# Performance work log

Measured on AMD Instinct MI355X. Metric: run time of the kernel, lower is better.

Reference implementation:

```python
import jax, jax.numpy as jnp
import numpy as np
from jax.ops import segment_sum, segment_max

N, E = 50000, 500000
D_IN, D_H, D_OUT = 128, 256, 40
BN_EPS = 1e-5


def setup_inputs() -> dict:
    key = jax.random.key(0)
    ks = jax.random.split(key, 16)
    g = lambda k, shape, fan: jax.random.normal(k, shape, jnp.float32) * (1.0 / np.sqrt(fan))
    inp = {
        "x": jax.random.normal(ks[0], (N, D_IN), jnp.float32),
        "edge_index": jax.random.randint(ks[1], (2, E), 0, N, jnp.int64),
        # GAT (heads=1)
        "W_gat": g(ks[2], (D_IN, D_H), D_IN),
        "att_src": g(ks[3], (D_H,), D_H),
        "att_dst": g(ks[4], (D_H,), D_H),
        "b_gat": jnp.zeros((D_H,), jnp.float32),
        # GIN MLP
        "W_gin1": g(ks[5], (D_IN, D_H), D_IN),
        "b_gin1": jnp.zeros((D_H,), jnp.float32),
        "W_gin2": g(ks[6], (D_H, D_H), D_H),
        "b_gin2": jnp.zeros((D_H,), jnp.float32),
        # GCN
        "W_gcn": g(ks[7], (D_IN, D_H), D_IN),
        "b_gcn": jnp.zeros((D_H,), jnp.float32),
        # BatchNorm1d(3*hidden)
        "gamma": jnp.ones((3 * D_H,), jnp.float32),
        "beta": jnp.zeros((3 * D_H,), jnp.float32),
        # head
        "W_lin": g(ks[8], (3 * D_H, D_H), 3 * D_H),
        "b_lin": jnp.zeros((D_H,), jnp.float32),
        "W_lin2": g(ks[9], (D_H, D_OUT), D_H),
        "b_lin2": jnp.zeros((D_OUT,), jnp.float32),
    }
    return inp


def _forward(x, edge_index, W_gat, att_src, att_dst, b_gat, W_gin1, b_gin1,
             W_gin2, b_gin2, W_gcn, b_gcn, gamma, beta, W_lin, b_lin, W_lin2, b_lin2):
    n = x.shape[0]
    src, dst = edge_index[0], edge_index[1]
    loop = jnp.arange(n, dtype=src.dtype)
    src_sl = jnp.concatenate([src, loop])  # edges + self-loops (GAT/GCN)
    dst_sl = jnp.concatenate([dst, loop])

    # ---- GATConv (1 head), messages src -> dst, softmax over dst ----
    xs = x @ W_gat                                   # [N, H]
    a = jax.nn.leaky_relu(xs @ att_src, negative_slope=0.2) if False else None
    e = (xs @ att_src)[src_sl] + (xs @ att_dst)[dst_sl]   # [E+N]
    e = jax.nn.leaky_relu(e, negative_slope=0.2)
    m = segment_max(e, dst_sl, num_segments=n)
    w = jnp.exp(e - m[dst_sl])
    denom = segment_sum(w, dst_sl, num_segments=n)
    alpha = w / denom[dst_sl]
    x_gat = segment_sum(alpha[:, None] * xs[src_sl], dst_sl, num_segments=n) + b_gat

    # ---- GINConv (eps=0): MLP(x + sum_neighbors x_j) ----
    agg = segment_sum(x[src], dst, num_segments=n)
    h = x + agg
    x_gin = jax.nn.relu(h @ W_gin1 + b_gin1) @ W_gin2 + b_gin2

    # ---- GCNConv: symmetric normalization with self-loops ----
    deg = segment_sum(jnp.ones_like(dst_sl, dtype=x.dtype), dst_sl, num_segments=n)
    dis = jax.lax.rsqrt(jnp.maximum(deg, 1.0))  # deg >= 1 due to self-loops
    norm = dis[src_sl] * dis[dst_sl]
    xw = x @ W_gcn
    x_gcn = segment_sum(norm[:, None] * xw[src_sl], dst_sl, num_segments=n) + b_gcn

    # ---- concat -> BN (training-mode batch stats) -> ReLU -> MLP head ----
    xc = jnp.concatenate([x_gat, x_gin, x_gcn], axis=1)  # [N, 3H]
    mu = jnp.mean(xc, axis=0)
    var = jnp.mean((xc - mu) ** 2, axis=0)
    xb = (xc - mu) * jax.lax.rsqrt(var + BN_EPS) * gamma + beta
    h2 = jax.nn.relu(jax.nn.relu(xb) @ W_lin + b_lin)
    return h2 @ W_lin2 + b_lin2


def reference(x, edge_index, W_gat, att_src, att_dst, b_gat, W_gin1, b_gin1,
              W_gin2, b_gin2, W_gcn, b_gcn, gamma, beta, W_lin, b_lin, W_lin2, b_lin2):
    return _forward(x, edge_index, W_gat, att_src, att_dst, b_gat, W_gin1, b_gin1,
                    W_gin2, b_gin2, W_gcn, b_gcn, gamma, beta, W_lin, b_lin, W_lin2, b_lin2)
```

## Files before the change

kernel.cpp:

```cpp
#include <hip/hip_runtime.h>
#include <math.h>

#define NN 50000
#define NE 500000
#define NRB 391

typedef __attribute__((ext_vector_type(8))) short short8;
typedef __attribute__((ext_vector_type(4))) float f32x4;

__device__ __forceinline__ float leaky02(float x) { return x > 0.f ? x : 0.2f * x; }
__device__ __forceinline__ ushort f2b(float f) {
    uint u = __float_as_uint(f);
    u += 0x7fffu + ((u >> 16) & 1u);
    return (ushort)(u >> 16);
}
__device__ __forceinline__ float b2f(ushort h) { return __uint_as_float(((uint)h) << 16); }
__device__ __forceinline__ float b2f_lo(uint w) { return __uint_as_float(w << 16); }
__device__ __forceinline__ float b2f_hi(uint w) { return __uint_as_float(w & 0xffff0000u); }
__device__ __forceinline__ uint pack2(float a, float b) {
    return (uint)f2b(a) | ((uint)f2b(b) << 16);
}

__global__ void mm_wt_all(const float* __restrict__ Wg, const float* __restrict__ Wi1,
                          const float* __restrict__ Wi2, const float* __restrict__ Wc,
                          const float* __restrict__ Wl,
                          ushort* __restrict__ tg, ushort* __restrict__ ti1,
                          ushort* __restrict__ ti2, ushort* __restrict__ tc,
                          ushort* __restrict__ tl)
{
    int idx = blockIdx.x * 256 + threadIdx.x;
    const float* W; ushort* T; int K; int base;
    if (idx < 32768)       { W = Wg;  T = tg;  K = 128; base = 0; }
    else if (idx < 65536)  { W = Wi1; T = ti1; K = 128; base = 32768; }
    else if (idx < 131072) { W = Wi2; T = ti2; K = 256; base = 65536; }
    else if (idx < 163840) { W = Wc;  T = tc;  K = 128; base = 131072; }
    else if (idx < 360448) { W = Wl;  T = tl;  K = 768; base = 163840; }
    else return;
    int i = idx - base;
    int n = i / K, k = i - n * K;
    T[i] = f2b(W[(size_t)k * 256 + n]);
}

__global__ void mm_attvec(const float* __restrict__ W, const float* __restrict__ as_,
                          const float* __restrict__ ad_, float* __restrict__ va, float* __restrict__ vd)
{
    int i = threadIdx.x;
    const float* vec = (i < 128) ? as_ : ad_;
    int k = i & 127;
    float s = 0.f;
    for (int j = 0; j < 256; ++j) s += W[(size_t)k * 256 + j] * vec[j];
    if (i < 128) va[k] = s; else vd[k] = s;
}

__global__ __launch_bounds__(256) void mm_cvt_es(const float* __restrict__ x,
                                                 const float* __restrict__ va, const float* __restrict__ vd,
                                                 ushort* __restrict__ xb,
                                                 float* __restrict__ es, float* __restrict__ ed)
{
    int node = blockIdx.x * 4 + (threadIdx.x >> 6);
    int lane = threadIdx.x & 63;
    if (node >= NN) return;
    float2 xv = *(const float2*)(x + (size_t)node * 128 + lane * 2);
    float2 a = *(const float2*)(va + lane * 2);
    float2 b = *(const float2*)(vd + lane * 2);
    *(uint*)(xb + (size_t)node * 128 + lane * 2) = pack2(xv.x, xv.y);
    float s = xv.x * a.x + xv.y * a.y;
    float d = xv.x * b.x + xv.y * b.y;
    #pragma unroll
    for (int off = 32; off; off >>= 1) {
        s += __shfl_down(s, off);
        d += __shfl_down(d, off);
    }
    if (lane == 0) { es[node] = s; ed[node] = d; }
}

__global__ void mm_count(const int* __restrict__ dst, int* __restrict__ deg)
{
    int e = blockIdx.x * 256 + threadIdx.x;
    if (e >= NE) return;
    atomicAdd(&deg[dst[e]], 1);
}

__global__ __launch_bounds__(256) void mm_scan1(const int* __restrict__ deg, int* __restrict__ part)
{
    __shared__ int red[256];
    int i = blockIdx.x * 256 + threadIdx.x;
    red[threadIdx.x] = (i < NN) ? deg[i] : 0;
    __syncthreads();
    for (int off = 128; off; off >>= 1) {
        if (threadIdx.x < off) red[threadIdx.x] += red[threadIdx.x + off];
        __syncthreads();
    }
    if (threadIdx.x == 0) part[blockIdx.x] = red[0];
}

__global__ __launch_bounds__(256) void mm_scan2(int* __restrict__ part, int nb)
{
    __shared__ int tile[256];
    int t = threadIdx.x;
    int v = (t < nb) ? part[t] : 0;
    tile[t] = v; __syncthreads();
    for (int off = 1; off < 256; off <<= 1) {
        int a = (t >= off) ? tile[t - off] : 0;
        __syncthreads();
        tile[t] += a;
        __syncthreads();
    }
    if (t < nb) part[t] = tile[t] - v;
}

__global__ __launch_bounds__(256) void mm_scan3(const int* __restrict__ deg, const int* __restrict__ part,
                                                int* __restrict__ row_ptr, int* __restrict__ cursor)
{
    __shared__ int tile[256];
    int t = threadIdx.x;
    int i = blockIdx.x * 256 + t;
    int v = (i < NN) ? deg[i] : 0;
    tile[t] = v; __syncthreads();
    for (int off = 1; off < 256; off <<= 1) {
        int a = (t >= off) ? tile[t - off] : 0;
        __syncthreads();
        tile[t] += a;
        __syncthreads();
    }
    if (i < NN) {
        int ex = part[blockIdx.x] + tile[t] - v;
        row_ptr[i] = ex;
        cursor[i] = ex;
    }
    if (i == 0) row_ptr[NN] = NE;
}

__global__ void mm_fill(const int* __restrict__ src, const int* __restrict__ dst,
                        int* __restrict__ cursor, int* __restrict__ csr_src)
{
    int e = blockIdx.x * 256 + threadIdx.x;
    if (e >= NE) return;
    int pos = atomicAdd(&cursor[dst[e]], 1);
    csr_src[pos] = src[e];
}

__global__ __launch_bounds__(256) void mm_sortseg(const int* __restrict__ row_ptr, int* __restrict__ csr_src)
{
    int d = blockIdx.x * 4 + (threadIdx.x >> 6);
    int lane = threadIdx.x & 63;
    if (d >= NN) return;
    int start = row_ptr[d], end = row_ptr[d + 1];
    int deg = end - start;
    if (deg <= 1 || deg > 64) return;
    int v = (start + lane < end) ? csr_src[start + lane] : 0x7fffffff;
    #pragma unroll
    for (int k = 2; k <= 64; k <<= 1) {
        #pragma unroll
        for (int j = k >> 1; j > 0; j >>= 1) {
            int o = __shfl_xor(v, j);
            bool asc = ((lane & k) == 0);
            bool low = ((lane & j) == 0);
            v = (asc == low) ? min(v, o) : max(v, o);
        }
    }
    if (start + lane < end) csr_src[start + lane] = v;
}

__global__ void mm_dis(const int* __restrict__ row_ptr, float* __restrict__ dis)
{
    int i = blockIdx.x * 256 + threadIdx.x;
    if (i >= NN) return;
    dis[i] = rsqrtf((float)(row_ptr[i + 1] - row_ptr[i] + 1));
}

__global__ __launch_bounds__(256) void mm_node_agg(
    const int* __restrict__ row_ptr, const int* __restrict__ csr_src,
    const float* __restrict__ es, const float* __restrict__ ed,
    const float* __restrict__ dis,
    const ushort* __restrict__ xb, ushort* __restrict__ aggb)
{
    int d = blockIdx.x * 4 + (threadIdx.x >> 6);
    int lane = threadIdx.x & 63;
    if (d >= NN) return;
    int start = row_ptr[d], end = row_ptr[d + 1];
    float edd = ed[d], disd = dis[d];
    float selfv = leaky02(es[d] + edd);

    int myidx = -1; float myl = -3.0e38f, mynw = 0.f;
    if (start + lane < end) {
        myidx = csr_src[start + lane];
        myl = leaky02(es[myidx] + edd);
        mynw = dis[myidx] * disd;
    }
    float lmax = fmaxf(selfv, myl);
    for (int e = start + 64 + lane; e < end; e += 64)
        lmax = fmaxf(lmax, leaky02(es[csr_src[e]] + edd));
    #pragma unroll
    for (int off = 1; off < 64; off <<= 1) lmax = fmaxf(lmax, __shfl_xor(lmax, off));
    float m = lmax;

    float lsum = (myidx >= 0) ? __expf(myl - m) : 0.f;
    if (lane == 0) lsum += __expf(selfv - m);
    for (int e = start + 64 + lane; e < end; e += 64)
        lsum += __expf(leaky02(es[csr_src[e]] + edd) - m);
    #pragma unroll
    for (int off = 1; off < 64; off <<= 1) lsum += __shfl_xor(lsum, off);
    float inv = 1.f / lsum;
    float myal = __expf(myl - m) * inv;

    float aself = __expf(selfv - m) * inv;
    float d2 = disd * disd;
    uint wself = *(const uint*)(xb + (size_t)d * 128 + lane * 2);
    float x0 = b2f_lo(wself), x1 = b2f_hi(wself);
    float gat0 = aself * x0, gat1 = aself * x1;
    float gin0 = x0, gin1 = x1;
    float gcn0 = d2 * x0, gcn1 = d2 * x1;

    for (int base = start; base < end; base += 64) {
        int cnt = min(64, end - base);
        int bidx; float bal, bnw;
        if (base == start) { bidx = myidx; bal = myal; bnw = mynw; }
        else {
            bidx = -1; bal = 0.f; bnw = 0.f;
            if (base + lane < end) {
                bidx = csr_src[base + lane];
                bal = __expf(leaky02(es[bidx] + edd) - m) * inv;
                bnw = dis[bidx] * disd;
            }
        }
        int j = 0;
        for (; j + 4 <= cnt; j += 4) {
            int   s0 = __shfl(bidx, j),     s1 = __shfl(bidx, j + 1);
            int   s2 = __shfl(bidx, j + 2), s3 = __shfl(bidx, j + 3);
            float a0 = __shfl(bal, j),      a1 = __shfl(bal, j + 1);
            float a2 = __shfl(bal, j + 2),  a3 = __shfl(bal, j + 3);
            float n0 = __shfl(bnw, j),      n1 = __shfl(bnw, j + 1);
            float n2 = __shfl(bnw, j + 2),  n3 = __shfl(bnw, j + 3);
            uint w0 = *(const uint*)(xb + (size_t)s0 * 128 + lane * 2);
            uint w1 = *(const uint*)(xb + (size_t)s1 * 128 + lane * 2);
            uint w2 = *(const uint*)(xb + (size_t)s2 * 128 + lane * 2);
            uint w3 = *(const uint*)(xb + (size_t)s3 * 128 + lane * 2);
            float p0, p1;
            p0 = b2f_lo(w0); p1 = b2f_hi(w0);
            gat0 += a0 * p0; gat1 += a0 * p1; gin0 += p0; gin1 += p1; gcn0 += n0 * p0; gcn1 += n0 * p1;
            p0 = b2f_lo(w1); p1 = b2f_hi(w1);
            gat0 += a1 * p0; gat1 += a1 * p1; gin0 += p0; gin1 += p1; gcn0 += n1 * p0; gcn1 += n1 * p1;
            p0 = b2f_lo(w2); p1 = b2f_hi(w2);
            gat0 += a2 * p0; gat1 += a2 * p1; gin0 += p0; gin1 += p1; gcn0 += n2 * p0; gcn1 += n2 * p1;
            p0 = b2f_lo(w3); p1 = b2f_hi(w3);
            gat0 += a3 * p0; gat1 += a3 * p1; gin0 += p0; gin1 += p1; gcn0 += n3 * p0; gcn1 += n3 * p1;
        }
        for (; j < cnt; ++j) {
            int   s0 = __shfl(bidx, j);
            float a0 = __shfl(bal, j);
            float n0 = __shfl(bnw, j);
            uint w0 = *(const uint*)(xb + (size_t)s0 * 128 + lane * 2);
            float p0 = b2f_lo(w0), p1 = b2f_hi(w0);
            gat0 += a0 * p0; gat1 += a0 * p1; gin0 += p0; gin1 += p1; gcn0 += n0 * p0; gcn1 += n0 * p1;
        }
    }
    ushort* orow = aggb + (size_t)d * 384;
    *(uint*)(orow + lane * 2)       = pack2(gat0, gat1);
    *(uint*)(orow + 128 + lane * 2) = pack2(gin0, gin1);
    *(uint*)(orow + 256 + lane * 2) = pack2(gcn0, gcn1);
}

__device__ __forceinline__ void gemm_core(
    const ushort* __restrict__ A, int lda, const ushort* __restrict__ Bt,
    const float* __restrict__ bias, float* __restrict__ pstat, int colbase,
    ushort* __restrict__ Cb, int ldc, int M, int K, int relu,
    ushort* lds)
{
    const int tid = threadIdx.x;
    const int wave = tid >> 6, lane = tid & 63;
    const int row0 = blockIdx.x * 128;
    const int col0 = blockIdx.y * 128;

    int arow0 = min(row0 + wave * 16 + (lane >> 2), M - 1);
    int arow1 = min(row0 + 64 + wave * 16 + (lane >> 2), M - 1);
    int brow0 = col0 + wave * 16 + (lane >> 2);
    int brow1 = col0 + 64 + wave * 16 + (lane >> 2);
    const ushort* pa0 = A + (size_t)arow0 * lda + (lane & 3) * 8;
    const ushort* pa1 = A + (size_t)arow1 * lda + (lane & 3) * 8;
    const ushort* pb0 = Bt + (size_t)brow0 * K + (lane & 3) * 8;
    const ushort* pb1 = Bt + (size_t)brow1 * K + (lane & 3) * 8;
    const int wr = (wave >> 1) * 64, wc = (wave & 1) * 64;

    f32x4 zero = {0.f, 0.f, 0.f, 0.f};
    f32x4 acc[4][4];
    #pragma unroll
    for (int m = 0; m < 4; ++m)
        #pragma unroll
        for (int n = 0; n < 4; ++n) acc[m][n] = zero;

    const int nt = K >> 5;

#define STAGE_C(bufi) { \
    ushort* Lb = lds + (bufi) * 8192; \
    __builtin_amdgcn_global_load_lds((const __attribute__((address_space(1))) void*)pa0, \
        (__attribute__((address_space(3))) void*)(Lb + wave * 512), 16, 0, 0); \
    __builtin_amdgcn_global_load_lds((const __attribute__((address_space(1))) void*)pa1, \
        (__attribute__((address_space(3))) void*)(Lb + 2048 + wave * 512), 16, 0, 0); \
    __builtin_amdgcn_global_load_lds((const __attribute__((address_space(1))) void*)pb0, \
        (__attribute__((address_space(3))) void*)(Lb + 4096 + wave * 512), 16, 0, 0); \
    __builtin_amdgcn_global_load_lds((const __attribute__((address_space(1))) void*)pb1, \
        (__attribute__((address_space(3))) void*)(Lb + 6144 + wave * 512), 16, 0, 0); \
    pa0 += 32; pa1 += 32; pb0 += 32; pb1 += 32; }

    STAGE_C(0);
    for (int t = 0; t < nt; ++t) {
        int cur = t & 1;
        if (t + 1 < nt) {
            STAGE_C(cur ^ 1);
            asm volatile("s_waitcnt vmcnt(4) lgkmcnt(0)" ::: "memory");
        } else {
            asm volatile("s_waitcnt vmcnt(0) lgkmcnt(0)" ::: "memory");
        }
        __builtin_amdgcn_s_barrier();
        const ushort* As = lds + cur * 8192;
        const ushort* Bs = As + 4096;
        short8 a[4], b[4];
        #pragma unroll
        for (int m = 0; m < 4; ++m)
            a[m] = *(const short8*)&As[(wr + m * 16 + (lane & 15)) * 32 + (lane >> 4) * 8];
        #pragma unroll
        for (int n = 0; n < 4; ++n)
            b[n] = *(const short8*)&Bs[(wc + n * 16 + (lane & 15)) * 32 + (lane >> 4) * 8];
        #pragma unroll
        for (int m = 0; m < 4; ++m)
            #pragma unroll
            for (int n = 0; n < 4; ++n)
                acc[m][n] = __builtin_amdgcn_mfma_f32_16x16x32_bf16(a[m], b[n], acc[m][n], 0, 0, 0);
        if (t + 1 < nt) __builtin_amdgcn_s_barrier();
    }
#undef STAGE_C

    #pragma unroll
    for (int n = 0; n < 4; ++n) {
        int col = col0 + wc + n * 16 + (lane & 15);
        float bb = bias ? bias[col] : 0.f;
        float s_acc = 0.f, q_acc = 0.f;
        #pragma unroll
        for (int m = 0; m < 4; ++m) {
            int rb = row0 + wr + m * 16 + (lane >> 4) * 4;
            #pragma unroll
            for (int r = 0; r < 4; ++r) {
                int row = rb + r;
                if (row < M) {
                    float v = acc[m][n][r] + bb;
                    if (relu) v = fmaxf(v, 0.f);
                    Cb[(size_t)row * ldc + col] = f2b(v);
                    s_acc += v; q_acc += v * v;
                }
            }
        }
        if (pstat) {
            s_acc += __shfl_xor(s_acc, 16); q_acc += __shfl_xor(q_acc, 16);
            s_acc += __shfl_xor(s_acc, 32); q_acc += __shfl_xor(q_acc, 32);
            if (lane < 16) {
                size_t slot = (size_t)(colbase + col) * NRB + blockIdx.x;
                unsafeAtomicAdd(&pstat[slot], s_acc);
                unsafeAtomicAdd(&pstat[(size_t)768 * NRB + slot], q_acc);
            }
        }
    }
}

__global__ __launch_bounds__(256) void mm_gemm3(
    const ushort* __restrict__ aggb,
    const ushort* __restrict__ wt_gat, const ushort* __restrict__ wt_gin1, const ushort* __restrict__ wt_gcn,
    const float* __restrict__ b_gat, const float* __restrict__ b_gin1, const float* __restrict__ b_gcn,
    float* __restrict__ pstat,
    ushort* __restrict__ xcb, ushort* __restrict__ hid_b)
{
    __shared__ ushort lds[16384];
    if (blockIdx.z == 0)
        gemm_core(aggb,       384, wt_gat,  b_gat,  pstat,   0,   xcb,       768, NN, 128, 0, lds);
    else if (blockIdx.z == 1)
        gemm_core(aggb + 128, 384, wt_gin1, b_gin1, nullptr, 0,   hid_b,     256, NN, 128, 1, lds);
    else
        gemm_core(aggb + 256, 384, wt_gcn,  b_gcn,  pstat,   512, xcb + 512, 768, NN, 128, 0, lds);
}

__global__ __launch_bounds__(256) void mm_gemm_bf(
    const ushort* __restrict__ A, int lda, const ushort* __restrict__ Bt,
    const float* __restrict__ bias, float* __restrict__ pstat, int colbase,
    ushort* __restrict__ Cb, int ldc, int M, int K, int relu)
{
    __shared__ ushort lds[16384];
    gemm_core(A, lda, Bt, bias, pstat, colbase, Cb, ldc, M, K, relu, lds);
}

__device__ __forceinline__ uint4 bn_relu_pack_l(uint4 w, const float* sc, const float* sh, int c)
{
    uint4 o;
    o.x = pack2(fmaxf(b2f_lo(w.x) * sc[c + 0] + sh[c + 0], 0.f), fmaxf(b2f_hi(w.x) * sc[c + 1] + sh[c + 1], 0.f));
    o.y = pack2(fmaxf(b2f_lo(w.y) * sc[c + 2] + sh[c + 2], 0.f), fmaxf(b2f_hi(w.y) * sc[c + 3] + sh[c + 3], 0.f));
    o.z = pack2(fmaxf(b2f_lo(w.z) * sc[c + 4] + sh[c + 4], 0.f), fmaxf(b2f_hi(w.z) * sc[c + 5] + sh[c + 5], 0.f));
    o.w = pack2(fmaxf(b2f_lo(w.w) * sc[c + 6] + sh[c + 6], 0.f), fmaxf(b2f_hi(w.w) * sc[c + 7] + sh[c + 7], 0.f));
    return o;
}

__global__ __launch_bounds__(256) void mm_gemm_bn(
    const ushort* __restrict__ A, const ushort* __restrict__ Bt,
    const float* __restrict__ bias,
    const float* __restrict__ sc, const float* __restrict__ sh,
    ushort* __restrict__ Cb, int ldc, int M)
{
    const int K = 768, lda = 768;
    __shared__ ushort lds[16384];
    __shared__ float sc_l[768], sh_l[768];
    const int tid = threadIdx.x;
    for (int i = tid; i < 768; i += 256) { sc_l[i] = sc[i]; sh_l[i] = sh[i]; }

    const int wave = tid >> 6, lane = tid & 63;
    const int row0 = blockIdx.x * 128;
    const int col0 = blockIdx.y * 128;

    int arow0 = min(row0 + wave * 16 + (lane >> 2), M - 1);
    int arow1 = min(row0 + 64 + wave * 16 + (lane >> 2), M - 1);
    int brow0 = col0 + wave * 16 + (lane >> 2);
    int brow1 = col0 + 64 + wave * 16 + (lane >> 2);
    const ushort* pa0 = A + (size_t)arow0 * lda + (lane & 3) * 8;
    const ushort* pa1 = A + (size_t)arow1 * lda + (lane & 3) * 8;
    const ushort* pb0 = Bt + (size_t)brow0 * K + (lane & 3) * 8;
    const ushort* pb1 = Bt + (size_t)brow1 * K + (lane & 3) * 8;
    const int wr = (wave >> 1) * 64, wc = (wave & 1) * 64;

    f32x4 zero = {0.f, 0.f, 0.f, 0.f};
    f32x4 acc[4][4];
    #pragma unroll
    for (int m = 0; m < 4; ++m)
        #pragma unroll
        for (int n = 0; n < 4; ++n) acc[m][n] = zero;

    const int nt = K >> 5;

#define STAGE_B(bufi) { \
    ushort* Lb = lds + (bufi) * 8192; \
    __builtin_amdgcn_global_load_lds((const __attribute__((address_space(1))) void*)pb0, \
        (__attribute__((address_space(3))) void*)(Lb + 4096 + wave * 512), 16, 0, 0); \
    __builtin_amdgcn_global_load_lds((const __attribute__((address_space(1))) void*)pb1, \
        (__attribute__((address_space(3))) void*)(Lb + 6144 + wave * 512), 16, 0, 0); \
    pb0 += 32; pb1 += 32; }

    uint4 w0 = *(const uint4*)pa0, w1 = *(const uint4*)pa1;
    pa0 += 32; pa1 += 32;
    STAGE_B(0);
    __syncthreads();
    {
        int c = (lane & 3) * 8;
        *(uint4*)(lds + wave * 512 + lane * 8) = bn_relu_pack_l(w0, sc_l, sh_l, c);
        *(uint4*)(lds + 2048 + wave * 512 + lane * 8) = bn_relu_pack_l(w1, sc_l, sh_l, c);
    }

    for (int t = 0; t < nt; ++t) {
        int cur = t & 1;
        bool more = (t + 1 < nt);
        uint4 w0n, w1n;
        if (more) {
            w0n = *(const uint4*)pa0; w1n = *(const uint4*)pa1;
            pa0 += 32; pa1 += 32;
            STAGE_B(cur ^ 1);
            asm volatile("s_waitcnt vmcnt(4) lgkmcnt(0)" ::: "memory");
        } else {
            asm volatile("s_waitcnt vmcnt(0) lgkmcnt(0)" ::: "memory");
        }
        __builtin_amdgcn_s_barrier();
        const ushort* As = lds + cur * 8192;
        const ushort* Bs = As + 4096;
        short8 a[4], b[4];
        #pragma unroll
        for (int m = 0; m < 4; ++m)
            a[m] = *(const short8*)&As[(wr + m * 16 + (lane & 15)) * 32 + (lane >> 4) * 8];
        #pragma unroll
        for (int n = 0; n < 4; ++n)
            b[n] = *(const short8*)&Bs[(wc + n * 16 + (lane & 15)) * 32 + (lane >> 4) * 8];
        #pragma unroll
        for (int m = 0; m < 4; ++m)
            #pragma unroll
            for (int n = 0; n < 4; ++n)
                acc[m][n] = __builtin_amdgcn_mfma_f32_16x16x32_bf16(a[m], b[n], acc[m][n], 0, 0, 0);
        if (more) {
            int c = (t + 1) * 32 + (lane & 3) * 8;
            ushort* Ln = lds + (cur ^ 1) * 8192;
            *(uint4*)(Ln + wave * 512 + lane * 8) = bn_relu_pack_l(w0n, sc_l, sh_l, c);
            *(uint4*)(Ln + 2048 + wave * 512 + lane * 8) = bn_relu_pack_l(w1n, sc_l, sh_l, c);
            __builtin_amdgcn_s_barrier();
        }
    }
#undef STAGE_B

    #pragma unroll
    for (int n = 0; n < 4; ++n) {
        int col = col0 + wc + n * 16 + (lane & 15);
        float bb = bias[col];
        #pragma unroll
        for (int m = 0; m < 4; ++m) {
            int rb = row0 + wr + m * 16 + (lane >> 4) * 4;
            #pragma unroll
            for (int r = 0; r < 4; ++r) {
                int row = rb + r;
                if (row < M)
                    Cb[(size_t)row * ldc + col] = f2b(fmaxf(acc[m][n][r] + bb, 0.f));
            }
        }
    }
}

__global__ void mm_bn_fin(const float* __restrict__ pstat, const float* __restrict__ gamma,
                          const float* __restrict__ beta,
                          float* __restrict__ scale, float* __restrict__ shift)
{
    int c = blockIdx.x * 256 + threadIdx.x;
    if (c >= 768) return;
    const float* ps = pstat + (size_t)c * NRB;
    const float* pq = pstat + (size_t)768 * NRB + (size_t)c * NRB;
    float s = 0.f, q = 0.f;
    for (int rb = 0; rb < NRB; ++rb) { s += ps[rb]; q += pq[rb]; }
    float invn = 1.f / (float)NN;
    float mu = s * invn;
    float ex2 = q * invn;
    float var = fmaxf(ex2 - mu * mu, 0.f);
    float rs = rsqrtf(var + 1e-5f);
    float sc = gamma[c] * rs;
    scale[c] = sc;
    shift[c] = beta[c] - mu * sc;
}

__global__ __launch_bounds__(256) void mm_head2(const ushort* __restrict__ h2b, const float* __restrict__ W2,
                                                const float* __restrict__ b2, float* __restrict__ out)
{
    __shared__ float Ws[256 * 40];
    for (int i = threadIdx.x; i < 256 * 40; i += 256) Ws[i] = W2[i];
    __syncthreads();
    int row = blockIdx.x * 32 + (threadIdx.x >> 3);
    int cg = (threadIdx.x & 7) * 5;
    if (row >= NN) return;
    const ushort* hr = h2b + (size_t)row * 256;
    float acc[5] = {0, 0, 0, 0, 0};
    for (int k = 0; k < 256; k += 8) {
        uint4 w = *(const uint4*)(hr + k);
        float a0 = b2f_lo(w.x), a1 = b2f_hi(w.x), a2 = b2f_lo(w.y), a3 = b2f_hi(w.y);
        float a4 = b2f_lo(w.z), a5 = b2f_hi(w.z), a6 = b2f_lo(w.w), a7 = b2f_hi(w.w);
        #pragma unroll
        for (int j = 0; j < 5; ++j) {
            acc[j] += a0 * Ws[(k + 0) * 40 + cg + j] + a1 * Ws[(k + 1) * 40 + cg + j]
                    + a2 * Ws[(k + 2) * 40 + cg + j] + a3 * Ws[(k + 3) * 40 + cg + j]
                    + a4 * Ws[(k + 4) * 40 + cg + j] + a5 * Ws[(k + 5) * 40 + cg + j]
                    + a6 * Ws[(k + 6) * 40 + cg + j] + a7 * Ws[(k + 7) * 40 + cg + j];
        }
    }
    #pragma unroll
    for (int j = 0; j < 5; ++j) out[(size_t)row * 40 + cg + j] = acc[j] + b2[cg + j];
}

extern "C" void kernel_launch(void* const* d_in, const int* in_sizes, int n_in,
                              void* d_out, int out_size, void* d_ws, size_t ws_size,
                              hipStream_t stream)
{
    const float* x      = (const float*)d_in[0];
    const int*   ei     = (const int*)d_in[1];
    const float* W_gat  = (const float*)d_in[2];
    const float* att_s  = (const float*)d_in[3];
    const float* att_d  = (const float*)d_in[4];
    const float* b_gat  = (const float*)d_in[5];
    const float* W_gin1 = (const float*)d_in[6];
    const float* b_gin1 = (const float*)d_in[7];
    const float* W_gin2 = (const float*)d_in[8];
    const float* b_gin2 = (const float*)d_in[9];
    const float* W_gcn  = (const float*)d_in[10];
    const float* b_gcn  = (const float*)d_in[11];
    const float* gamma  = (const float*)d_in[12];
    const float* beta   = (const float*)d_in[13];
    const float* W_lin  = (const float*)d_in[14];
    const float* b_lin  = (const float*)d_in[15];
    const float* W_lin2 = (const float*)d_in[16];
    const float* b_lin2 = (const float*)d_in[17];
    const int* src = ei;
    const int* dst = ei + NE;
    float* out = (float*)d_out;

    float* ws = (float*)d_ws;
    size_t off = 0;
    ushort* xb      = (ushort*)(ws + off); off += (size_t)NN * 64;
    ushort* aggb    = (ushort*)(ws + off); off += (size_t)NN * 192;
    ushort* hid_b   = (ushort*)(ws + off); off += (size_t)NN * 128;
    ushort* xcb     = (ushort*)(ws + off); off += (size_t)NN * 384;
    float* es       = ws + off; off += NN;
    float* ed       = ws + off; off += NN;
    float* dis      = ws + off; off += NN;
    float* va       = ws + off; off += 128;
    float* vd       = ws + off; off += 128;
    float* pstat    = ws + off; off += (size_t)1536 * NRB;
    float* bscale   = ws + off; off += 768;
    float* bshift   = ws + off; off += 768;
    ushort* wt_gat  = (ushort*)(ws + off); off += 128 * 256 / 2;
    ushort* wt_gin1 = (ushort*)(ws + off); off += 128 * 256 / 2;
    ushort* wt_gin2 = (ushort*)(ws + off); off += 256 * 256 / 2;
    ushort* wt_gcn  = (ushort*)(ws + off); off += 128 * 256 / 2;
    ushort* wt_lin  = (ushort*)(ws + off); off += 768 * 256 / 2;
    int* part       = (int*)(ws + off); off += 256;
    int* row_ptr    = (int*)(ws + off); off += NN + 1;
    int* cursor     = (int*)(ws + off); off += NN;
    int* csr_src    = (int*)(ws + off); off += NE;

    dim3 blk(256);
    dim3 gemm_grid(NRB, 2);
    dim3 gemm_grid3(NRB, 2, 3);
    const int NB = (NN + 255) / 256;

    hipMemsetAsync(pstat, 0, (size_t)1536 * NRB * sizeof(float), stream);
    hipMemsetAsync(cursor, 0, NN * sizeof(int), stream);

    mm_wt_all<<<(360448 + 255) / 256, blk, 0, stream>>>(W_gat, W_gin1, W_gin2, W_gcn, W_lin,
                                                        wt_gat, wt_gin1, wt_gin2, wt_gcn, wt_lin);
    mm_attvec<<<1, blk, 0, stream>>>(W_gat, att_s, att_d, va, vd);

    mm_cvt_es<<<(NN + 3) / 4, blk, 0, stream>>>(x, va, vd, xb, es, ed);

    mm_count<<<(NE + 255) / 256, blk, 0, stream>>>(dst, cursor);
    mm_scan1<<<NB, blk, 0, stream>>>(cursor, part);
    mm_scan2<<<1, blk, 0, stream>>>(part, NB);
    mm_scan3<<<NB, blk, 0, stream>>>(cursor, part, row_ptr, cursor);
    mm_dis<<<(NN + 255) / 256, blk, 0, stream>>>(row_ptr, dis);
    mm_fill<<<(NE + 255) / 256, blk, 0, stream>>>(src, dst, cursor, csr_src);
    mm_sortseg<<<(NN + 3) / 4, blk, 0, stream>>>(row_ptr, csr_src);

    mm_node_agg<<<(NN + 3) / 4, blk, 0, stream>>>(row_ptr, csr_src, es, ed, dis, xb, aggb);

    mm_gemm3<<<gemm_grid3, blk, 0, stream>>>(aggb, wt_gat, wt_gin1, wt_gcn,
                                             b_gat, b_gin1, b_gcn, pstat, xcb, hid_b);
    mm_gemm_bf<<<gemm_grid, blk, 0, stream>>>(hid_b, 256, wt_gin2, b_gin2, pstat, 256,
                                              xcb + 256, 768, NN, 256, 0);

    mm_bn_fin<<<3, blk, 0, stream>>>(pstat, gamma, beta, bscale, bshift);

    mm_gemm_bn<<<gemm_grid, blk, 0, stream>>>(xcb, wt_lin, b_lin, bscale, bshift, hid_b, 256, NN);
    mm_head2<<<(NN + 31) / 32, blk, 0, stream>>>(hid_b, W_lin2, b_lin2, out);
}
```

Baseline: 418.9 us.

## Fuse neighbor sort into aggregation and replace BN stat atomics with LDS reduction

The per-segment bitonic sort of CSR source indices now runs in registers inside the node aggregation kernel, which removes a separate launch and one read-write pass over csr_src. In the GEMM epilogue, per-column BN sums are reduced across the two row-half waves in shared memory and written once per block with plain stores. This drops the atomics and the pstat memset. The partial-stat layout changes to row-block-major, and the finalize kernel now reads it with a stride of 768. Segments with more than 64 neighbors are no longer written back sorted, but the sort only affects summation order.

After: 383.1 us. -8.6%, faster.

```diff
diff --git a/kernel.cpp b/kernel.cpp
--- a/kernel.cpp
+++ b/kernel.cpp
@@ -140,51 +140,42 @@
     csr_src[pos] = src[e];
 }
 
-__global__ __launch_bounds__(256) void mm_sortseg(const int* __restrict__ row_ptr, int* __restrict__ csr_src)
+__global__ void mm_dis(const int* __restrict__ row_ptr, float* __restrict__ dis)
+{
+    int i = blockIdx.x * 256 + threadIdx.x;
+    if (i >= NN) return;
+    dis[i] = rsqrtf((float)(row_ptr[i + 1] - row_ptr[i] + 1));
+}
+
+__global__ __launch_bounds__(256) void mm_node_agg(
+    const int* __restrict__ row_ptr, const int* __restrict__ csr_src,
+    const float* __restrict__ es, const float* __restrict__ ed,
+    const float* __restrict__ dis,
+    const ushort* __restrict__ xb, ushort* __restrict__ aggb)
 {
     int d = blockIdx.x * 4 + (threadIdx.x >> 6);
     int lane = threadIdx.x & 63;
     if (d >= NN) return;
     int start = row_ptr[d], end = row_ptr[d + 1];
     int deg = end - start;
-    if (deg <= 1 || deg > 64) return;
-    int v = (start + lane < end) ? csr_src[start + lane] : 0x7fffffff;
-    #pragma unroll
-    for (int k = 2; k <= 64; k <<= 1) {
-        #pragma unroll
-        for (int j = k >> 1; j > 0; j >>= 1) {
-            int o = __shfl_xor(v, j);
-            bool asc = ((lane & k) == 0);
-            bool low = ((lane & j) == 0);
-            v = (asc == low) ? min(v, o) : max(v, o);
-        }
-    }
-    if (start + lane < end) csr_src[start + lane] = v;
-}
-
-__global__ void mm_dis(const int* __restrict__ row_ptr, float* __restrict__ dis)
-{
-    int i = blockIdx.x * 256 + threadIdx.x;
-    if (i >= NN) return;
-    dis[i] = rsqrtf((float)(row_ptr[i + 1] - row_ptr[i] + 1));
-}
-
-__global__ __launch_bounds__(256) void mm_node_agg(
-    const int* __restrict__ row_ptr, const int* __restrict__ csr_src,
-    const float* __restrict__ es, const float* __restrict__ ed,
-    const float* __restrict__ dis,
-    const ushort* __restrict__ xb, ushort* __restrict__ aggb)
-{
-    int d = blockIdx.x * 4 + (threadIdx.x >> 6);
-    int lane = threadIdx.x & 63;
-    if (d >= NN) return;
-    int start = row_ptr[d], end = row_ptr[d + 1];
     float edd = ed[d], disd = dis[d];
     float selfv = leaky02(es[d] + edd);
 
-    int myidx = -1; float myl = -3.0e38f, mynw = 0.f;
-    if (start + lane < end) {
-        myidx = csr_src[start + lane];
+    int myidx = (start + lane < end) ? csr_src[start + lane] : 0x7fffffff;
+    if (deg <= 64) {
+        #pragma unroll
+        for (int k = 2; k <= 64; k <<= 1) {
+            #pragma unroll
+            for (int j = k >> 1; j > 0; j >>= 1) {
+                int o = __shfl_xor(myidx, j);
+                bool keepmin = (((lane & k) == 0) == ((lane & j) == 0));
+                myidx = keepmin ? min(myidx, o) : max(myidx, o);
+            }
+        }
+    }
+    bool valid = (lane < deg);
+    float myl = -3.0e38f, mynw = 0.f;
+    if (valid) {
         myl = leaky02(es[myidx] + edd);
         mynw = dis[myidx] * disd;
     }
@@ -195,7 +186,7 @@
     for (int off = 1; off < 64; off <<= 1) lmax = fmaxf(lmax, __shfl_xor(lmax, off));
     float m = lmax;
 
-    float lsum = (myidx >= 0) ? __expf(myl - m) : 0.f;
+    float lsum = valid ? __expf(myl - m) : 0.f;
     if (lane == 0) lsum += __expf(selfv - m);
     for (int e = start + 64 + lane; e < end; e += 64)
         lsum += __expf(leaky02(es[csr_src[e]] + edd) - m);
@@ -265,7 +256,7 @@
     const ushort* __restrict__ A, int lda, const ushort* __restrict__ Bt,
     const float* __restrict__ bias, float* __restrict__ pstat, int colbase,
     ushort* __restrict__ Cb, int ldc, int M, int K, int relu,
-    ushort* lds)
+    ushort* lds, float* sred)
 {
     const int tid = threadIdx.x;
     const int wave = tid >> 6, lane = tid & 63;
@@ -354,11 +345,19 @@
             s_acc += __shfl_xor(s_acc, 16); q_acc += __shfl_xor(q_acc, 16);
             s_acc += __shfl_xor(s_acc, 32); q_acc += __shfl_xor(q_acc, 32);
             if (lane < 16) {
-                size_t slot = (size_t)(colbase + col) * NRB + blockIdx.x;
-                unsafeAtomicAdd(&pstat[slot], s_acc);
-                unsafeAtomicAdd(&pstat[(size_t)768 * NRB + slot], q_acc);
+                int cl = wc + n * 16 + (lane & 15);
+                int half = wave >> 1;
+                sred[half * 128 + cl] = s_acc;
+                sred[256 + half * 128 + cl] = q_acc;
             }
         }
+    }
+    if (pstat) {
+        __syncthreads();
+        int c = tid & 127, which = tid >> 7;
+        float v = sred[which * 256 + c] + sred[which * 256 + 128 + c];
+        size_t gcol = (size_t)(colbase + col0 + c);
+        pstat[(which ? (size_t)NRB * 768 : 0) + (size_t)blockIdx.x * 768 + gcol] = v;
     }
 }
 
@@ -370,12 +369,13 @@
     ushort* __restrict__ xcb, ushort* __restrict__ hid_b)
 {
     __shared__ ushort lds[16384];
+    __shared__ float sred[512];
     if (blockIdx.z == 0)
-        gemm_core(aggb,       384, wt_gat,  b_gat,  pstat,   0,   xcb,       768, NN, 128, 0, lds);
+        gemm_core(aggb,       384, wt_gat,  b_gat,  pstat,   0,   xcb,       768, NN, 128, 0, lds, sred);
     else if (blockIdx.z == 1)
-        gemm_core(aggb + 128, 384, wt_gin1, b_gin1, nullptr, 0,   hid_b,     256, NN, 128, 1, lds);
+        gemm_core(aggb + 128, 384, wt_gin1, b_gin1, nullptr, 0,   hid_b,     256, NN, 128, 1, lds, sred);
     else
-        gemm_core(aggb + 256, 384, wt_gcn,  b_gcn,  pstat,   512, xcb + 512, 768, NN, 128, 0, lds);
+        gemm_core(aggb + 256, 384, wt_gcn,  b_gcn,  pstat,   512, xcb + 512, 768, NN, 128, 0, lds, sred);
 }
 
 __global__ __launch_bounds__(256) void mm_gemm_bf(
@@ -384,7 +384,8 @@
     ushort* __restrict__ Cb, int ldc, int M, int K, int relu)
 {
     __shared__ ushort lds[16384];
-    gemm_core(A, lda, Bt, bias, pstat, colbase, Cb, ldc, M, K, relu, lds);
+    __shared__ float sred[512];
+    gemm_core(A, lda, Bt, bias, pstat, colbase, Cb, ldc, M, K, relu, lds, sred);
 }
 
 __device__ __forceinline__ uint4 bn_relu_pack_l(uint4 w, const float* sc, const float* sh, int c)
@@ -510,10 +511,13 @@
 {
     int c = blockIdx.x * 256 + threadIdx.x;
     if (c >= 768) return;
-    const float* ps = pstat + (size_t)c * NRB;
-    const float* pq = pstat + (size_t)768 * NRB + (size_t)c * NRB;
+    const float* ps = pstat + c;
+    const float* pq = pstat + (size_t)NRB * 768 + c;
     float s = 0.f, q = 0.f;
-    for (int rb = 0; rb < NRB; ++rb) { s += ps[rb]; q += pq[rb]; }
+    for (int rb = 0; rb < NRB; ++rb) {
+        s += ps[(size_t)rb * 768];
+        q += pq[(size_t)rb * 768];
+    }
     float invn = 1.f / (float)NN;
     float mu = s * invn;
     float ex2 = q * invn;
@@ -606,7 +610,6 @@
     dim3 gemm_grid3(NRB, 2, 3);
     const int NB = (NN + 255) / 256;
 
-    hipMemsetAsync(pstat, 0, (size_t)1536 * NRB * sizeof(float), stream);
     hipMemsetAsync(cursor, 0, NN * sizeof(int), stream);
 
     mm_wt_all<<<(360448 + 255) / 256, blk, 0, stream>>>(W_gat, W_gin1, W_gin2, W_gcn, W_lin,
@@ -621,7 +624,6 @@
     mm_scan3<<<NB, blk, 0, stream>>>(cursor, part, row_ptr, cursor);
     mm_dis<<<(NN + 255) / 256, blk, 0, stream>>>(row_ptr, dis);
     mm_fill<<<(NE + 255) / 256, blk, 0, stream>>>(src, dst, cursor, csr_src);
-    mm_sortseg<<<(NN + 3) / 4, blk, 0, stream>>>(row_ptr, csr_src);
 
     mm_node_agg<<<(NN + 3) / 4, blk, 0, stream>>>(row_ptr, csr_src, es, ed, dis, xb, aggb);
 
```
